# Optimization experiments

Measured on AMD Instinct MI355X. Metric: run time of the kernel, lower is better.

Reference implementation:

```python
import jax, jax.numpy as jnp
import numpy as np

B, N_CITY, EC, VOCAB = 4096, 50, 128, 40000


def setup_inputs() -> dict:
    key = jax.random.key(0)
    k1, k2, k3, k4 = jax.random.split(key, 4)
    x = jax.random.normal(k1, (B, EC), dtype=jnp.float32)
    top_city_emb = jax.random.normal(k2, (B, N_CITY, EC), dtype=jnp.float32)
    top_city_id = jax.random.randint(k3, (B, N_CITY), 0, VOCAB)
    prob = jnp.zeros((B, VOCAB), dtype=jnp.float32)
    # nn.Linear(EC, EC) params
    W = jax.random.normal(k4, (EC, EC), dtype=jnp.float32) * (1.0 / np.sqrt(EC))
    b = jnp.zeros((EC,), dtype=jnp.float32)
    return {"x": x, "top_city_emb": top_city_emb, "top_city_id": top_city_id,
            "prob": prob, "W": W, "b": b}


def reference(x, top_city_emb, top_city_id, prob, W, b):
    # Linear projection (torch Linear: x @ W^T + b)
    emb_pred = x @ W.T + b                                  # [B, EC]
    # Broadcast dot-product score against candidate embeddings
    scores = jnp.einsum('be,bne->bn', emb_pred, top_city_emb)  # [B, N_CITY]
    p = jax.nn.softmax(scores, axis=1)                      # [B, N_CITY]
    # Scatter-add softmax probs into the vocab-sized output
    rows = jnp.arange(p.shape[0])[:, None]                  # [B, 1] -> broadcast to [B, N_CITY]
    rows = jnp.broadcast_to(rows, top_city_id.shape)
    out = jnp.zeros_like(prob).at[rows, top_city_id].add(p) + 1e-6
    return out
```

## Files before the change

kernel.cpp:

```cpp
#include <hip/hip_runtime.h>
#include <hip/hip_bf16.h>

#define NC    50
#define EC    128
#define VOCAB 40000

__global__ __launch_bounds__(256)
void EmbDotSoftMax_fill_kernel(float4* __restrict__ out4)
{
    const float4 fv = make_float4(1e-6f, 1e-6f, 1e-6f, 1e-6f);
    const long stride = 5000L * 1024;
    long base = (long)blockIdx.x * 1024 + threadIdx.x;
    #pragma unroll 4
    for (int it = 0; it < 8; ++it, base += stride) {
        out4[base      ] = fv;
        out4[base + 256] = fv;
        out4[base + 512] = fv;
        out4[base + 768] = fv;
    }
}

__global__ __launch_bounds__(128)
void EmbDotSoftMax_scatter_kernel(const float* __restrict__ x,
                                  const float* __restrict__ emb,
                                  const int*   __restrict__ ids,
                                  const float* __restrict__ W,
                                  const float* __restrict__ bias,
                                  float*       __restrict__ out)
{
    const int b   = blockIdx.x;
    const int tid = threadIdx.x;
    const int w   = tid >> 6;
    const int l   = tid & 63;

    __shared__ float pred_s[EC];
    __shared__ float scores_s[NC];

    float* out_row = out + (size_t)b * VOCAB;

    {
        const float x0 = x[(size_t)b * EC + l];
        const float x1 = x[(size_t)b * EC + 64 + l];
        const float* Wbase = W + (size_t)w * 64 * EC;
        float mine = 0.0f;
        #pragma unroll 8
        for (int i = 0; i < 64; ++i) {
            const float* row = Wbase + i * EC;
            float part = fmaf(x0, row[l], x1 * row[l + 64]);
            #pragma unroll
            for (int off = 32; off; off >>= 1)
                part += __shfl_xor(part, off);
            if (i == l) mine = part;
        }
        pred_s[w * 64 + l] = mine + bias[w * 64 + l];
    }
    __syncthreads();

    {
        const float p0 = pred_s[l];
        const float p1 = pred_s[l + 64];
        const float* base = emb + (size_t)b * NC * EC + (size_t)w * (NC / 2) * EC;

        float part[NC / 2];
        #pragma unroll
        for (int i = 0; i < NC / 2; ++i) {
            const float* er = base + i * EC;
            part[i] = fmaf(p0, er[l], p1 * er[l + 64]);
        }
        #pragma unroll
        for (int off = 32; off; off >>= 1) {
            #pragma unroll
            for (int i = 0; i < NC / 2; ++i)
                part[i] += __shfl_xor(part[i], off);
        }
        if (l == 0) {
            #pragma unroll
            for (int i = 0; i < NC / 2; ++i)
                scores_s[w * (NC / 2) + i] = part[i];
        }
    }
    __syncthreads();

    if (tid < NC) {
        float m = -1e30f;
        #pragma unroll
        for (int n = 0; n < NC; ++n) m = fmaxf(m, scores_s[n]);
        float sum = 0.0f;
        #pragma unroll
        for (int n = 0; n < NC; ++n) sum += __expf(scores_s[n] - m);
        const float p  = __expf(scores_s[tid] - m) / sum;
        const int   id = ids[(size_t)b * NC + tid];
        atomicAdd(out_row + id, p);
    }
}

extern "C" void kernel_launch(void* const* d_in, const int* in_sizes, int n_in,
                              void* d_out, int out_size, void* d_ws, size_t ws_size,
                              hipStream_t stream) {
    const float* x    = (const float*)d_in[0];
    const float* emb  = (const float*)d_in[1];
    const int*   ids  = (const int*)d_in[2];
    const float* W    = (const float*)d_in[4];
    const float* bias = (const float*)d_in[5];
    float*       out  = (float*)d_out;

    const int B = in_sizes[0] / EC;

    hipLaunchKernelGGL(EmbDotSoftMax_fill_kernel,
                       dim3(5000), dim3(256), 0, stream,
                       reinterpret_cast<float4*>(out));

    hipLaunchKernelGGL(EmbDotSoftMax_scatter_kernel,
                       dim3(B), dim3(128), 0, stream,
                       x, emb, ids, W, bias, out);
}
```

Baseline: 189.8 us.

## Pre-pack transposed W into workspace and use per-thread dot products

Adds a one-block kernel that writes W into a transposed float4-packed layout in the workspace. The scatter kernel then computes each output feature with one thread looping over float4 columns, and each candidate score with one thread, instead of wave-wide shuffle reductions. This removes the many shuffle reductions in both the projection and the score step. In exchange it adds an extra launch, leaves only 50 of 128 threads active in the score step, and reads each emb row with strided per-thread float4 loads. The original kernel is kept as a fallback when the workspace is too small.

New measurement: 188.3 us. No clear change (-0.8%).

```diff
diff --git a/kernel.cpp b/kernel.cpp
--- a/kernel.cpp
+++ b/kernel.cpp
@@ -4,6 +4,19 @@
 #define NC    50
 #define EC    128
 #define VOCAB 40000
+
+__global__ __launch_bounds__(256)
+void EmbDotSoftMax_wtpack_kernel(const float* __restrict__ W,
+                                 float4*      __restrict__ WTp)
+{
+    const int t = threadIdx.x;
+    #pragma unroll
+    for (int idx = t; idx < (EC / 4) * EC; idx += 256) {
+        const int k4 = idx >> 7;
+        const int e  = idx & 127;
+        WTp[idx] = reinterpret_cast<const float4*>(W)[e * (EC / 4) + k4];
+    }
+}
 
 __global__ __launch_bounds__(256)
 void EmbDotSoftMax_fill_kernel(float4* __restrict__ out4)
@@ -21,23 +34,91 @@
 }
 
 __global__ __launch_bounds__(128)
-void EmbDotSoftMax_scatter_kernel(const float* __restrict__ x,
-                                  const float* __restrict__ emb,
-                                  const int*   __restrict__ ids,
-                                  const float* __restrict__ W,
-                                  const float* __restrict__ bias,
-                                  float*       __restrict__ out)
+void EmbDotSoftMax_scatter_kernel(const float*  __restrict__ x,
+                                  const float*  __restrict__ emb,
+                                  const int*    __restrict__ ids,
+                                  const float4* __restrict__ WTp,
+                                  const float*  __restrict__ bias,
+                                  float*        __restrict__ out)
+{
+    const int b   = blockIdx.x;
+    const int tid = threadIdx.x;
+
+    __shared__ float4 x_s4[EC / 4];
+    __shared__ float  pred_s[EC];
+    __shared__ float  score_s[NC];
+
+    float* out_row = out + (size_t)b * VOCAB;
+
+    if (tid < EC / 4)
+        x_s4[tid] = reinterpret_cast<const float4*>(x + (size_t)b * EC)[tid];
+    __syncthreads();
+
+    {
+        float acc = 0.0f;
+        #pragma unroll
+        for (int k4 = 0; k4 < EC / 4; ++k4) {
+            const float4 w  = WTp[k4 * EC + tid];
+            const float4 xv = x_s4[k4];
+            acc = fmaf(w.x, xv.x, acc);
+            acc = fmaf(w.y, xv.y, acc);
+            acc = fmaf(w.z, xv.z, acc);
+            acc = fmaf(w.w, xv.w, acc);
+        }
+        pred_s[tid] = acc + bias[tid];
+    }
+    __syncthreads();
+
+    {
+        const int w = tid >> 6;
+        const int l = tid & 63;
+        if (l < NC / 2) {
+            const int n = w * (NC / 2) + l;
+            const float4* er =
+                reinterpret_cast<const float4*>(emb + ((size_t)b * NC + n) * EC);
+            float acc = 0.0f;
+            #pragma unroll
+            for (int j = 0; j < EC / 4; ++j) {
+                const float4 e4 = er[j];
+                const float4 p4 = reinterpret_cast<const float4*>(pred_s)[j];
+                acc = fmaf(e4.x, p4.x, acc);
+                acc = fmaf(e4.y, p4.y, acc);
+                acc = fmaf(e4.z, p4.z, acc);
+                acc = fmaf(e4.w, p4.w, acc);
+            }
+            score_s[n] = acc;
+        }
+    }
+    __syncthreads();
+
+    if (tid < NC) {
+        float m = -1e30f;
+        #pragma unroll
+        for (int n = 0; n < NC; ++n) m = fmaxf(m, score_s[n]);
+        float sum = 0.0f;
+        #pragma unroll
+        for (int n = 0; n < NC; ++n) sum += __expf(score_s[n] - m);
+        const float p  = __expf(score_s[tid] - m) / sum;
+        const int   id = ids[(size_t)b * NC + tid];
+        atomicAdd(out_row + id, p);
+    }
+}
+
+__global__ __launch_bounds__(128)
+void EmbDotSoftMax_scatter_fb(const float* __restrict__ x,
+                              const float* __restrict__ emb,
+                              const int*   __restrict__ ids,
+                              const float* __restrict__ W,
+                              const float* __restrict__ bias,
+                              float*       __restrict__ out)
 {
     const int b   = blockIdx.x;
     const int tid = threadIdx.x;
     const int w   = tid >> 6;
     const int l   = tid & 63;
-
     __shared__ float pred_s[EC];
     __shared__ float scores_s[NC];
-
     float* out_row = out + (size_t)b * VOCAB;
-
     {
         const float x0 = x[(size_t)b * EC + l];
         const float x1 = x[(size_t)b * EC + 64 + l];
@@ -55,12 +136,10 @@
         pred_s[w * 64 + l] = mine + bias[w * 64 + l];
     }
     __syncthreads();
-
     {
         const float p0 = pred_s[l];
         const float p1 = pred_s[l + 64];
         const float* base = emb + (size_t)b * NC * EC + (size_t)w * (NC / 2) * EC;
-
         float part[NC / 2];
         #pragma unroll
         for (int i = 0; i < NC / 2; ++i) {
@@ -80,7 +159,6 @@
         }
     }
     __syncthreads();
-
     if (tid < NC) {
         float m = -1e30f;
         #pragma unroll
@@ -88,9 +166,8 @@
         float sum = 0.0f;
         #pragma unroll
         for (int n = 0; n < NC; ++n) sum += __expf(scores_s[n] - m);
-        const float p  = __expf(scores_s[tid] - m) / sum;
-        const int   id = ids[(size_t)b * NC + tid];
-        atomicAdd(out_row + id, p);
+        const float p = __expf(scores_s[tid] - m) / sum;
+        atomicAdd(out_row + ids[(size_t)b * NC + tid], p);
     }
 }
 
@@ -105,12 +182,24 @@
     float*       out  = (float*)d_out;
 
     const int B = in_sizes[0] / EC;
-
-    hipLaunchKernelGGL(EmbDotSoftMax_fill_kernel,
-                       dim3(5000), dim3(256), 0, stream,
-                       reinterpret_cast<float4*>(out));
-
-    hipLaunchKernelGGL(EmbDotSoftMax_scatter_kernel,
-                       dim3(B), dim3(128), 0, stream,
-                       x, emb, ids, W, bias, out);
-}
+    const size_t ws_needed = (size_t)(EC / 4) * EC * sizeof(float4);
+
+    if (ws_size >= ws_needed) {
+        float4* WTp = (float4*)d_ws;
+        hipLaunchKernelGGL(EmbDotSoftMax_wtpack_kernel,
+                           dim3(1), dim3(256), 0, stream, W, WTp);
+        hipLaunchKernelGGL(EmbDotSoftMax_fill_kernel,
+                           dim3(5000), dim3(256), 0, stream,
+                           reinterpret_cast<float4*>(out));
+        hipLaunchKernelGGL(EmbDotSoftMax_scatter_kernel,
+                           dim3(B), dim3(128), 0, stream,
+                           x, emb, ids, WTp, bias, out);
+    } else {
+        hipLaunchKernelGGL(EmbDotSoftMax_fill_kernel,
+                           dim3(5000), dim3(256), 0, stream,
+                           reinterpret_cast<float4*>(out));
+        hipLaunchKernelGGL(EmbDotSoftMax_scatter_fb,
+                           dim3(B), dim3(128), 0, stream,
+                           x, emb, ids, W, bias, out);
+    }
+}
```
